# Performance work log

Measured on AMD Instinct MI355X. Metric: run time of the kernel, lower is better.

## Reference

```python
import jax, jax.numpy as jnp
import numpy as np


def setup_inputs() -> dict:
    key = jax.random.key(0)
    k1, k2, k3 = jax.random.split(key, 3)
    B, IN, H, OUT = 2048, 4096, 4096, 1024
    x = jax.random.normal(k1, (B, IN), dtype=jnp.float32)
    fc1_weight = jax.random.randint(k2, (H, IN), 0, 2).astype(jnp.int32)
    fc2_weight = jax.random.randint(k3, (OUT, H), 0, 2).astype(jnp.int32)
    return {"x": x, "fc1_weight": fc1_weight, "fc2_weight": fc2_weight, "threshold": 2048}


def _binary_popcount_matmul(a, w):
    # a: (B, K) in {0,1}, w: (N, K) in {0,1}
    # matches = sum_k 1 - (a XOR w) = a@w.T + (1-a)@(1-w).T  (identical math,
    # avoids materializing the (B, N, K) XNOR tensor the naive code builds)
    return jnp.einsum('bk,nk->bn', a, w) + jnp.einsum('bk,nk->bn', 1 - a, 1 - w)


def reference(x, fc1_weight, fc2_weight, threshold):
    xb = (x.reshape(x.shape[0], -1) >= 0).astype(jnp.int32)   # binarize input
    pc1 = _binary_popcount_matmul(xb, fc1_weight)              # (B, H) popcounts
    act1 = (pc1 >= threshold).astype(jnp.int32)                # threshold activation
    pc2 = _binary_popcount_matmul(act1, fc2_weight)            # (B, OUT) popcounts
    return pc2
```

## Files before the change

### kernel.cpp

```cpp
#include <hip/hip_runtime.h>
#include <stdint.h>

typedef int v4i  __attribute__((ext_vector_type(4)));
typedef int v16i __attribute__((ext_vector_type(16)));

__device__ __forceinline__ void gload_lds16(const void* g, void* l) {
    __builtin_amdgcn_global_load_lds(
        (const __attribute__((address_space(1))) void*)g,
        (__attribute__((address_space(3))) void*)l, 16, 0, 0);
}

__device__ __forceinline__ v4i gload16(const int8_t* p) {
    v4i r;
    asm volatile("global_load_dwordx4 %0, %1, off" : "=v"(r) : "v"(p) : "memory");
    return r;
}

template<typename T, bool ISFLOAT>
__global__ __launch_bounds__(512)
void pack_frag(const T* __restrict__ in, int8_t* __restrict__ F, int K) {
    __shared__ int8_t lbuf[32 * 1040];
    const int t  = threadIdx.x;
    const int db = blockIdx.y;
    const int c0 = blockIdx.x << 10;

    #pragma unroll
    for (int p = 0; p < 16; ++p) {
        int idx = p * 512 + t;
        int row = idx >> 8, c4 = idx & 255;
        uint32_t b;
        if constexpr (ISFLOAT) {
            const float4 v = *(const float4*)(in + (size_t)(db * 32 + row) * K + c0 + c4 * 4);
            b =  (v.x >= 0.0f ? 0x01u : 0xFFu)
              | ((v.y >= 0.0f ? 0x01u : 0xFFu) << 8)
              | ((v.z >= 0.0f ? 0x01u : 0xFFu) << 16)
              | ((v.w >= 0.0f ? 0x01u : 0xFFu) << 24);
        } else {
            const int4 v = *(const int4*)(in + (size_t)(db * 32 + row) * K + c0 + c4 * 4);
            b =  (v.x ? 0x01u : 0xFFu)
              | ((v.y ? 0x01u : 0xFFu) << 8)
              | ((v.z ? 0x01u : 0xFFu) << 16)
              | ((v.w ? 0x01u : 0xFFu) << 24);
        }
        *(uint32_t*)(lbuf + row * 1040 + c4 * 4) = b;
    }
    __syncthreads();

    const int s  = t >> 4;
    const int l0 = (t & 15) * 4;
    const int KC = K >> 5;
    int8_t* dst = F + ((size_t)db * KC + blockIdx.x * 32 + s) * 1024;
    #pragma unroll
    for (int li = 0; li < 4; ++li) {
        int l = l0 + li;
        uint4 v = *(const uint4*)(lbuf + (l & 31) * 1040 + s * 32 + (l >> 5) * 16);
        *(uint4*)(dst + l * 16) = v;
    }
}

__global__ __launch_bounds__(256, 2)
void bnn_l1_areg(const int8_t* __restrict__ Af,
                 const int8_t* __restrict__ Bf,
                 const int* __restrict__ thr_ptr,
                 int8_t* __restrict__ actf)
{
    constexpr int KC  = 128;
    constexpr int NKT = 64;

    __shared__ int8_t lds[4 * 8192];

    const int tid  = threadIdx.x;
    const int lane = tid & 63;
    const int wv   = tid >> 6;
    const int wr   = wv >> 1, wc = wv & 1;

    const int g   = blockIdx.x;
    const int idx = g >> 3;
    const int bn  = (g & 7) * 4 + (idx >> 4);
    const int bm  = idx & 15;

    const int8_t* gB0; const int8_t* gB1;
    uint32_t lo0, lo1;
    {
        int s0 = tid;
        gB0 = Bf + ((size_t)(bn * 4 + (s0 >> 7)) * KC + ((s0 >> 6) & 1)) * 1024 + (s0 & 63) * 16;
        lo0 = (uint32_t)s0 * 16;
        int s1 = tid + 256;
        gB1 = Bf + ((size_t)(bn * 4 + (s1 >> 7)) * KC + ((s1 >> 6) & 1)) * 1024 + (s1 & 63) * 16;
        lo1 = (uint32_t)s1 * 16;
    }

    const int8_t* gA = Af + ((size_t)(bm * 4 + wr * 2) * KC) * 1024 + lane * 16;

    v16i acc[2][2];
    #pragma unroll
    for (int i = 0; i < 2; ++i)
        #pragma unroll
        for (int j = 0; j < 2; ++j) acc[i][j] = {};

    v4i Ab[4][4];

    #pragma unroll
    for (int p = 0; p < 3; ++p) {
        const int8_t* ga = gA + p * 2048;
        Ab[p][0] = gload16(ga);
        Ab[p][1] = gload16(ga + 1024);
        Ab[p][2] = gload16(ga + 131072);
        Ab[p][3] = gload16(ga + 132096);
        gload_lds16(gB0, lds + p * 8192 + lo0); gB0 += 2048;
        gload_lds16(gB1, lds + p * 8192 + lo1); gB1 += 2048;
    }

#define KT_BODY(KT, P)                                                         \
    {                                                                          \
        const int kt_ = (KT);                                                  \
        if (kt_ < NKT - 2)      asm volatile("s_waitcnt vmcnt(12)" ::: "memory"); \
        else if (kt_ == NKT - 2) asm volatile("s_waitcnt vmcnt(6)"  ::: "memory"); \
        else                     asm volatile("s_waitcnt vmcnt(0)"  ::: "memory"); \
        __builtin_amdgcn_sched_barrier(0);                                     \
        __builtin_amdgcn_s_barrier();                                          \
        __builtin_amdgcn_sched_barrier(0);                                     \
        const int8_t* Bb = lds + (P) * 8192 + wc * 4096 + lane * 16;           \
        v4i bf00 = *(const v4i*)(Bb + 0);                                      \
        v4i bf10 = *(const v4i*)(Bb + 2048);                                   \
        v4i bf01 = *(const v4i*)(Bb + 1024);                                   \
        v4i bf11 = *(const v4i*)(Bb + 3072);                                   \
        if (kt_ + 3 < NKT) {                                                   \
            const int8_t* ga = gA + (kt_ + 3) * 2048;                          \
            Ab[((P)+3)&3][0] = gload16(ga);                                    \
            Ab[((P)+3)&3][1] = gload16(ga + 1024);                             \
            Ab[((P)+3)&3][2] = gload16(ga + 131072);                           \
            Ab[((P)+3)&3][3] = gload16(ga + 132096);                           \
            gload_lds16(gB0, lds + (((P)+3)&3) * 8192 + lo0); gB0 += 2048;     \
            gload_lds16(gB1, lds + (((P)+3)&3) * 8192 + lo1); gB1 += 2048;     \
        }                                                                      \
        __builtin_amdgcn_sched_barrier(0);                                     \
        asm volatile("s_waitcnt lgkmcnt(0)" ::: "memory");                     \
        __builtin_amdgcn_sched_barrier(0);                                     \
        __builtin_amdgcn_s_setprio(1);                                         \
        acc[0][0] = __builtin_amdgcn_mfma_i32_32x32x32_i8(Ab[P][0], bf00, acc[0][0], 0, 0, 0); \
        acc[0][1] = __builtin_amdgcn_mfma_i32_32x32x32_i8(Ab[P][0], bf10, acc[0][1], 0, 0, 0); \
        acc[1][0] = __builtin_amdgcn_mfma_i32_32x32x32_i8(Ab[P][2], bf00, acc[1][0], 0, 0, 0); \
        acc[1][1] = __builtin_amdgcn_mfma_i32_32x32x32_i8(Ab[P][2], bf10, acc[1][1], 0, 0, 0); \
        acc[0][0] = __builtin_amdgcn_mfma_i32_32x32x32_i8(Ab[P][1], bf01, acc[0][0], 0, 0, 0); \
        acc[0][1] = __builtin_amdgcn_mfma_i32_32x32x32_i8(Ab[P][1], bf11, acc[0][1], 0, 0, 0); \
        acc[1][0] = __builtin_amdgcn_mfma_i32_32x32x32_i8(Ab[P][3], bf01, acc[1][0], 0, 0, 0); \
        acc[1][1] = __builtin_amdgcn_mfma_i32_32x32x32_i8(Ab[P][3], bf11, acc[1][1], 0, 0, 0); \
        __builtin_amdgcn_s_setprio(0);                                         \
        __builtin_amdgcn_sched_barrier(0);                                     \
    }

    #pragma unroll 1
    for (int kt0 = 0; kt0 < NKT; kt0 += 4) {
        KT_BODY(kt0 + 0, 0)
        KT_BODY(kt0 + 1, 1)
        KT_BODY(kt0 + 2, 2)
        KT_BODY(kt0 + 3, 3)
    }
#undef KT_BODY

    __syncthreads();
    const int thr = *thr_ptr;
    int8_t* bits = lds;
    #pragma unroll
    for (int i = 0; i < 2; ++i)
        #pragma unroll
        for (int j = 0; j < 2; ++j) {
            int dimb = wr * 64 + i * 32 + 4 * (lane >> 5);
            int gcl  = wc * 64 + j * 32 + (lane & 31);
            #pragma unroll
            for (int reg = 0; reg < 16; ++reg) {
                int dl = dimb + (reg & 3) + 8 * (reg >> 2);
                int match = (4096 + acc[i][j][reg]) >> 1;
                bits[dl * 144 + gcl] = (match >= thr) ? (int8_t)1 : (int8_t)-1;
            }
        }
    __syncthreads();
    const int s    = tid >> 4;
    const int dblk = s >> 2, kcl = s & 3;
    const int l0   = (tid & 15) * 4;
    int8_t* dst = actf + ((size_t)(bm * 4 + dblk) * KC + bn * 4 + kcl) * 1024;
    #pragma unroll
    for (int li = 0; li < 4; ++li) {
        int l = l0 + li;
        uint4 v = *(const uint4*)(bits + (dblk * 32 + (l & 31)) * 144
                                       + kcl * 32 + (l >> 5) * 16);
        *(uint4*)(dst + l * 16) = v;
    }
}

template<int WN>
__global__ __launch_bounds__(256, 1)
void bnn_mfma2(const int8_t* __restrict__ Af,
               const int8_t* __restrict__ Bf,
               int* __restrict__ out, int Nout)
{
    constexpr int KC     = 128;
    constexpr int NKT    = 64;
    constexpr int NBB    = 2 * WN;
    constexpr int ASLOTS = 512;
    constexpr int BSLOTS = 128 * NBB;
    constexpr int SLOTS  = ASLOTS + BSLOTS;
    constexpr int NLD    = SLOTS / 256;
    constexpr uint32_t BUFSZ = (uint32_t)SLOTS * 16;

    __shared__ int8_t lds[3][SLOTS * 16];

    const int tid  = threadIdx.x;
    const int lane = tid & 63;
    const int wv   = tid >> 6;
    const int wr   = wv >> 1, wc = wv & 1;

    const int g   = blockIdx.x;
    const int idx = g >> 3;
    const int bn  = (g & 7) * 2 + (idx >> 4);
    const int bm  = idx & 15;

    const int8_t* gsrc[NLD];
    uint32_t ldoff[NLD];
    #pragma unroll
    for (int i = 0; i < NLD; ++i) {
        int sbase = wv * 64 + 256 * i;
        ldoff[i] = (uint32_t)sbase * 16;
        const int8_t* base;
        if (sbase < ASLOTS) {
            int R = sbase >> 7, C = (sbase >> 6) & 1;
            base = Af + ((size_t)(bm * 4 + R) * KC + C) * 1024;
        } else {
            int s = sbase - ASLOTS;
            int R = s >> 7, C = (s >> 6) & 1;
            base = Bf + ((size_t)(bn * NBB + R) * KC + C) * 1024;
        }
        gsrc[i] = base + lane * 16;
    }

    auto stage = [&](int buf) {
        #pragma unroll
        for (int i = 0; i < NLD; ++i) {
            gload_lds16(gsrc[i], (int8_t*)lds + (uint32_t)buf * BUFSZ + ldoff[i]);
            gsrc[i] += 2048;
        }
    };

    v16i acc[2][WN];
    #pragma unroll
    for (int i = 0; i < 2; ++i)
        #pragma unroll
        for (int j = 0; j < WN; ++j) acc[i][j] = {};

    stage(0);
    stage(1);

    int cur = 0, nxt = 2;
    #pragma unroll 1
    for (int kt = 0; kt < NKT; ++kt) {
        if (kt < NKT - 1) asm volatile("s_waitcnt vmcnt(3)" ::: "memory");
        else              asm volatile("s_waitcnt vmcnt(0)" ::: "memory");
        __builtin_amdgcn_sched_barrier(0);
        __builtin_amdgcn_s_barrier();
        __builtin_amdgcn_sched_barrier(0);

        if (kt < NKT - 2) {
            stage(nxt);
            nxt = (nxt == 2) ? 0 : nxt + 1;
        }

        const int8_t* Al = lds[cur];
        const int8_t* Bl = lds[cur] + ASLOTS * 16;
        #pragma unroll
        for (int kc = 0; kc < 2; ++kc) {
            v4i af[2], bf[WN];
            #pragma unroll
            for (int i = 0; i < 2; ++i)
                af[i] = *(const v4i*)(Al + (((wr * 2 + i) * 2 + kc) * 64 + lane) * 16);
            #pragma unroll
            for (int j = 0; j < WN; ++j)
                bf[j] = *(const v4i*)(Bl + (((wc * WN + j) * 2 + kc) * 64 + lane) * 16);
            #pragma unroll
            for (int i = 0; i < 2; ++i)
                #pragma unroll
                for (int j = 0; j < WN; ++j)
                    acc[i][j] = __builtin_amdgcn_mfma_i32_32x32x32_i8(af[i], bf[j], acc[i][j], 0, 0, 0);
        }
        cur = (cur == 2) ? 0 : cur + 1;
    }

    #pragma unroll
    for (int i = 0; i < 2; ++i)
        #pragma unroll
        for (int j = 0; j < WN; ++j) {
            int gc = bn * (64 * WN) + wc * (32 * WN) + j * 32 + (lane & 31);
            #pragma unroll
            for (int reg = 0; reg < 16; ++reg) {
                int gr = bm * 128 + wr * 64 + i * 32
                       + (reg & 3) + 8 * (reg >> 2) + 4 * (lane >> 5);
                out[(size_t)gr * Nout + gc] = (4096 + acc[i][j][reg]) >> 1;
            }
        }
}

extern "C" void kernel_launch(void* const* d_in, const int* in_sizes, int n_in,
                              void* d_out, int out_size, void* d_ws, size_t ws_size,
                              hipStream_t stream) {
    const float* x   = (const float*)d_in[0];
    const int*   w1  = (const int*)d_in[1];
    const int*   w2  = (const int*)d_in[2];
    const int*   thr = (const int*)d_in[3];
    int* out = (int*)d_out;

    const int B = 2048, IN = 4096, H = 4096, OUT = 1024;
    uint8_t* ws = (uint8_t*)d_ws;

    int8_t* Af  = (int8_t*)(ws);
    int8_t* W1f = (int8_t*)(ws + ((size_t)8  << 20));
    int8_t* W2f = (int8_t*)(ws + ((size_t)24 << 20));
    int8_t* Act = (int8_t*)(ws + ((size_t)28 << 20));

    pack_frag<float, true ><<<dim3(IN / 1024, B   / 32), 512, 0, stream>>>(x,  Af,  IN);
    pack_frag<int,   false><<<dim3(IN / 1024, H   / 32), 512, 0, stream>>>(w1, W1f, IN);
    pack_frag<int,   false><<<dim3(H  / 1024, OUT / 32), 512, 0, stream>>>(w2, W2f, H);

    bnn_l1_areg<<<512, 256, 0, stream>>>(Af, W1f, thr, Act);
    bnn_mfma2<1><<<256, 256, 0, stream>>>(Act, W2f, out, OUT);
}
```

Measured before the change: 91.43 us.

## Load layer-1 B fragments directly into registers instead of via LDS

```diff
diff --git a/kernel.cpp b/kernel.cpp
--- a/kernel.cpp
+++ b/kernel.cpp
@@ -59,7 +59,7 @@
 }
 
 __global__ __launch_bounds__(256, 2)
-void bnn_l1_areg(const int8_t* __restrict__ Af,
+void bnn_l1_flow(const int8_t* __restrict__ Af,
                  const int8_t* __restrict__ Bf,
                  const int* __restrict__ thr_ptr,
                  int8_t* __restrict__ actf)
@@ -67,7 +67,7 @@
     constexpr int KC  = 128;
     constexpr int NKT = 64;
 
-    __shared__ int8_t lds[4 * 8192];
+    __shared__ int8_t bits[128 * 144];
 
     const int tid  = threadIdx.x;
     const int lane = tid & 63;
@@ -79,18 +79,8 @@
     const int bn  = (g & 7) * 4 + (idx >> 4);
     const int bm  = idx & 15;
 
-    const int8_t* gB0; const int8_t* gB1;
-    uint32_t lo0, lo1;
-    {
-        int s0 = tid;
-        gB0 = Bf + ((size_t)(bn * 4 + (s0 >> 7)) * KC + ((s0 >> 6) & 1)) * 1024 + (s0 & 63) * 16;
-        lo0 = (uint32_t)s0 * 16;
-        int s1 = tid + 256;
-        gB1 = Bf + ((size_t)(bn * 4 + (s1 >> 7)) * KC + ((s1 >> 6) & 1)) * 1024 + (s1 & 63) * 16;
-        lo1 = (uint32_t)s1 * 16;
-    }
-
     const int8_t* gA = Af + ((size_t)(bm * 4 + wr * 2) * KC) * 1024 + lane * 16;
+    const int8_t* gB = Bf + ((size_t)(bn * 4 + wc * 2) * KC) * 1024 + lane * 16;
 
     v16i acc[2][2];
     #pragma unroll
@@ -98,7 +88,7 @@
         #pragma unroll
         for (int j = 0; j < 2; ++j) acc[i][j] = {};
 
-    v4i Ab[4][4];
+    v4i Ab[4][4], Bb[4][4];
 
     #pragma unroll
     for (int p = 0; p < 3; ++p) {
@@ -107,45 +97,41 @@
         Ab[p][1] = gload16(ga + 1024);
         Ab[p][2] = gload16(ga + 131072);
         Ab[p][3] = gload16(ga + 132096);
-        gload_lds16(gB0, lds + p * 8192 + lo0); gB0 += 2048;
-        gload_lds16(gB1, lds + p * 8192 + lo1); gB1 += 2048;
+        const int8_t* gb = gB + p * 2048;
+        Bb[p][0] = gload16(gb);
+        Bb[p][1] = gload16(gb + 1024);
+        Bb[p][2] = gload16(gb + 131072);
+        Bb[p][3] = gload16(gb + 132096);
     }
 
 #define KT_BODY(KT, P)                                                         \
     {                                                                          \
         const int kt_ = (KT);                                                  \
-        if (kt_ < NKT - 2)      asm volatile("s_waitcnt vmcnt(12)" ::: "memory"); \
-        else if (kt_ == NKT - 2) asm volatile("s_waitcnt vmcnt(6)"  ::: "memory"); \
+        if (kt_ < NKT - 2)       asm volatile("s_waitcnt vmcnt(16)" ::: "memory"); \
+        else if (kt_ == NKT - 2) asm volatile("s_waitcnt vmcnt(8)"  ::: "memory"); \
         else                     asm volatile("s_waitcnt vmcnt(0)"  ::: "memory"); \
         __builtin_amdgcn_sched_barrier(0);                                     \
-        __builtin_amdgcn_s_barrier();                                          \
-        __builtin_amdgcn_sched_barrier(0);                                     \
-        const int8_t* Bb = lds + (P) * 8192 + wc * 4096 + lane * 16;           \
-        v4i bf00 = *(const v4i*)(Bb + 0);                                      \
-        v4i bf10 = *(const v4i*)(Bb + 2048);                                   \
-        v4i bf01 = *(const v4i*)(Bb + 1024);                                   \
-        v4i bf11 = *(const v4i*)(Bb + 3072);                                   \
         if (kt_ + 3 < NKT) {                                                   \
             const int8_t* ga = gA + (kt_ + 3) * 2048;                          \
             Ab[((P)+3)&3][0] = gload16(ga);                                    \
             Ab[((P)+3)&3][1] = gload16(ga + 1024);                             \
             Ab[((P)+3)&3][2] = gload16(ga + 131072);                           \
             Ab[((P)+3)&3][3] = gload16(ga + 132096);                           \
-            gload_lds16(gB0, lds + (((P)+3)&3) * 8192 + lo0); gB0 += 2048;     \
-            gload_lds16(gB1, lds + (((P)+3)&3) * 8192 + lo1); gB1 += 2048;     \
+            const int8_t* gb = gB + (kt_ + 3) * 2048;                          \
+            Bb[((P)+3)&3][0] = gload16(gb);                                    \
+            Bb[((P)+3)&3][1] = gload16(gb + 1024);                             \
+            Bb[((P)+3)&3][2] = gload16(gb + 131072);                           \
+            Bb[((P)+3)&3][3] = gload16(gb + 132096);                           \
         }                                                                      \
-        __builtin_amdgcn_sched_barrier(0);                                     \
-        asm volatile("s_waitcnt lgkmcnt(0)" ::: "memory");                     \
-        __builtin_amdgcn_sched_barrier(0);                                     \
         __builtin_amdgcn_s_setprio(1);                                         \
-        acc[0][0] = __builtin_amdgcn_mfma_i32_32x32x32_i8(Ab[P][0], bf00, acc[0][0], 0, 0, 0); \
-        acc[0][1] = __builtin_amdgcn_mfma_i32_32x32x32_i8(Ab[P][0], bf10, acc[0][1], 0, 0, 0); \
-        acc[1][0] = __builtin_amdgcn_mfma_i32_32x32x32_i8(Ab[P][2], bf00, acc[1][0], 0, 0, 0); \
-        acc[1][1] = __builtin_amdgcn_mfma_i32_32x32x32_i8(Ab[P][2], bf10, acc[1][1], 0, 0, 0); \
-        acc[0][0] = __builtin_amdgcn_mfma_i32_32x32x32_i8(Ab[P][1], bf01, acc[0][0], 0, 0, 0); \
-        acc[0][1] = __builtin_amdgcn_mfma_i32_32x32x32_i8(Ab[P][1], bf11, acc[0][1], 0, 0, 0); \
-        acc[1][0] = __builtin_amdgcn_mfma_i32_32x32x32_i8(Ab[P][3], bf01, acc[1][0], 0, 0, 0); \
-        acc[1][1] = __builtin_amdgcn_mfma_i32_32x32x32_i8(Ab[P][3], bf11, acc[1][1], 0, 0, 0); \
+        acc[0][0] = __builtin_amdgcn_mfma_i32_32x32x32_i8(Ab[P][0], Bb[P][0], acc[0][0], 0, 0, 0); \
+        acc[0][1] = __builtin_amdgcn_mfma_i32_32x32x32_i8(Ab[P][0], Bb[P][2], acc[0][1], 0, 0, 0); \
+        acc[1][0] = __builtin_amdgcn_mfma_i32_32x32x32_i8(Ab[P][2], Bb[P][0], acc[1][0], 0, 0, 0); \
+        acc[1][1] = __builtin_amdgcn_mfma_i32_32x32x32_i8(Ab[P][2], Bb[P][2], acc[1][1], 0, 0, 0); \
+        acc[0][0] = __builtin_amdgcn_mfma_i32_32x32x32_i8(Ab[P][1], Bb[P][1], acc[0][0], 0, 0, 0); \
+        acc[0][1] = __builtin_amdgcn_mfma_i32_32x32x32_i8(Ab[P][1], Bb[P][3], acc[0][1], 0, 0, 0); \
+        acc[1][0] = __builtin_amdgcn_mfma_i32_32x32x32_i8(Ab[P][3], Bb[P][1], acc[1][0], 0, 0, 0); \
+        acc[1][1] = __builtin_amdgcn_mfma_i32_32x32x32_i8(Ab[P][3], Bb[P][3], acc[1][1], 0, 0, 0); \
         __builtin_amdgcn_s_setprio(0);                                         \
         __builtin_amdgcn_sched_barrier(0);                                     \
     }
@@ -161,7 +147,6 @@
 
     __syncthreads();
     const int thr = *thr_ptr;
-    int8_t* bits = lds;
     #pragma unroll
     for (int i = 0; i < 2; ++i)
         #pragma unroll
@@ -320,6 +305,6 @@
     pack_frag<int,   false><<<dim3(IN / 1024, H   / 32), 512, 0, stream>>>(w1, W1f, IN);
     pack_frag<int,   false><<<dim3(H  / 1024, OUT / 32), 512, 0, stream>>>(w2, W2f, H);
 
-    bnn_l1_areg<<<512, 256, 0, stream>>>(Af, W1f, thr, Act);
+    bnn_l1_flow<<<512, 256, 0, stream>>>(Af, W1f, thr, Act);
     bnn_mfma2<1><<<256, 256, 0, stream>>>(Act, W2f, out, OUT);
 }
```

After: 100.2 us. +9.6%, slower.
